# Kernel optimization log

Hardware: AMD Instinct MI355X
Metric: run time of the kernel (lower is better)

## Reference

```python
import jax, jax.numpy as jnp
import numpy as np

MARGIN = 0.3
N = 16384


def setup_inputs() -> dict:
    key = jax.random.key(0)
    k1, k2 = jax.random.split(key)
    inputs = jax.random.normal(k1, (N,), dtype=jnp.float32)
    targets = jax.random.randint(k2, (N,), 0, 2, dtype=jnp.int64)
    return {"inputs": inputs, "targets": targets}


def reference(inputs, targets):
    # Original: a = inputs[targets==1], b = inputs[targets==0];
    # all pairs (i, j): MarginRankingLoss(sigmoid(a_i), sigmoid(b_j), y=1)
    #   = mean_ij relu(margin - (sigmoid(a_i) - sigmoid(b_j)))
    # Expressed as a masked N x N broadcast so shapes stay static (jit-safe).
    s = jax.nn.sigmoid(inputs)  # [N]
    pos = (targets == 1)        # anchors-positive side
    neg = (targets == 0)        # negative side
    # hinge[i, j] = relu(margin - (s_i - s_j)) for pos i, neg j
    hinge = jax.nn.relu(MARGIN - (s[:, None] - s[None, :]))  # [N, N]
    mask = pos[:, None] & neg[None, :]                        # [N, N]
    num_pairs = jnp.sum(pos) * jnp.sum(neg)
    total = jnp.sum(jnp.where(mask, hinge, 0.0))
    return total / num_pairs.astype(s.dtype)
```

## Files before the change

### kernel.cpp

```cpp
#include <hip/hip_runtime.h>
#include <hip/hip_bf16.h>
#include <math.h>

#define MARGIN 0.3f
#define PAIR_BLOCKS 512


__global__ __launch_bounds__(256) void prep_compact_kernel(
        const float* __restrict__ inputs,
        const int* __restrict__ targets,
        float* __restrict__ a,
        float* __restrict__ b,
        unsigned int* __restrict__ pos_count,
        unsigned int* __restrict__ neg_count,
        int n) {
    __shared__ unsigned int wPos[4], wNeg[4];
    __shared__ unsigned int basePos, baseNeg;
    const int tid = threadIdx.x;
    const int i = blockIdx.x * 256 + tid;
    const bool valid = (i < n);
    float x = valid ? inputs[i] : 0.0f;
    int t = valid ? targets[i] : -1;
    float s = 1.0f / (1.0f + expf(-x));
    bool isPos = valid && (t == 1);
    bool isNeg = valid && (t == 0);

    unsigned long long mP = __ballot(isPos);
    unsigned long long mN = __ballot(isNeg);
    int lane = tid & 63, wave = tid >> 6;
    unsigned long long below = (1ull << lane) - 1ull;
    unsigned int pPre = (unsigned int)__popcll(mP & below);
    unsigned int nPre = (unsigned int)__popcll(mN & below);
    if (lane == 0) { wPos[wave] = (unsigned int)__popcll(mP);
                     wNeg[wave] = (unsigned int)__popcll(mN); }
    __syncthreads();
    if (tid == 0) {
        unsigned int tp = wPos[0] + wPos[1] + wPos[2] + wPos[3];
        unsigned int tn = wNeg[0] + wNeg[1] + wNeg[2] + wNeg[3];
        basePos = atomicAdd(pos_count, tp);
        baseNeg = atomicAdd(neg_count, tn);
    }
    __syncthreads();
    unsigned int wOffP = 0, wOffN = 0;
    for (int w = 0; w < wave; w++) { wOffP += wPos[w]; wOffN += wNeg[w]; }
    if (isPos) a[basePos + wOffP + pPre] = s;
    if (isNeg) b[baseNeg + wOffN + nPre] = MARGIN + s;
}

__global__ __launch_bounds__(256) void pair_reduce_kernel(
        const float* __restrict__ a,
        const float* __restrict__ b,
        const unsigned int* __restrict__ pos_count,
        const unsigned int* __restrict__ neg_count,
        double* __restrict__ total,
        unsigned int* __restrict__ done,
        float* __restrict__ out) {
    const int tid = threadIdx.x;
    const unsigned int P = *pos_count;
    const unsigned int Q = *neg_count;
    const unsigned int tilesI = (P + 511u) / 512u;
    const unsigned int tilesJ = (Q + 255u) / 256u;
    const unsigned int numTiles = tilesI * tilesJ;

    __shared__ float4 bs4[64];
    __shared__ double wsum[4];
    float* bs = (float*)bs4;

    double dlocal = 0.0;

    for (unsigned int tile = blockIdx.x; tile < numTiles; tile += gridDim.x) {
        unsigned int ti = tile / tilesJ;
        unsigned int tj = tile - ti * tilesJ;

        unsigned int j = tj * 256u + tid;
        bs[tid] = (j < Q) ? b[j] : -1e30f;

        unsigned int i0 = ti * 512u + tid;
        float a0 = (i0        < P) ? a[i0]       : 1e30f;
        float a1 = (i0 + 256u < P) ? a[i0 + 256] : 1e30f;
        __syncthreads();

        float c0 = 0.0f, c1 = 0.0f;
        #pragma unroll 8
        for (int q4 = 0; q4 < 64; q4++) {
            float4 b4 = bs4[q4];
            c0 += fmaxf(b4.x - a0, 0.0f);
            c0 += fmaxf(b4.y - a0, 0.0f);
            c0 += fmaxf(b4.z - a0, 0.0f);
            c0 += fmaxf(b4.w - a0, 0.0f);
            c1 += fmaxf(b4.x - a1, 0.0f);
            c1 += fmaxf(b4.y - a1, 0.0f);
            c1 += fmaxf(b4.z - a1, 0.0f);
            c1 += fmaxf(b4.w - a1, 0.0f);
        }
        dlocal += (double)c0 + (double)c1;
        __syncthreads();
    }

    for (int off = 32; off > 0; off >>= 1)
        dlocal += __shfl_down(dlocal, off, 64);

    int lane = tid & 63, wave = tid >> 6;
    if (lane == 0) wsum[wave] = dlocal;
    __syncthreads();
    if (tid == 0) {
        double bsum = wsum[0] + wsum[1] + wsum[2] + wsum[3];
        atomicAdd(total, bsum);
        __threadfence();
        unsigned int prev = atomicAdd(done, 1u);
        if (prev == gridDim.x - 1) {
            __threadfence();
            double T = atomicAdd(total, 0.0);
            double PQ = (double)P * (double)Q;
            out[0] = (PQ > 0.0) ? (float)(T / PQ) : 0.0f;
        }
    }
}

extern "C" void kernel_launch(void* const* d_in, const int* in_sizes, int n_in,
                              void* d_out, int out_size, void* d_ws, size_t ws_size,
                              hipStream_t stream) {
    const float* inputs  = (const float*)d_in[0];
    const int*   targets = (const int*)d_in[1];
    float* out = (float*)d_out;
    int n = in_sizes[0];

    char* ws = (char*)d_ws;
    double*       total     = (double*)(ws + 0);
    unsigned int* pos_count = (unsigned int*)(ws + 8);
    unsigned int* neg_count = (unsigned int*)(ws + 12);
    unsigned int* done      = (unsigned int*)(ws + 16);
    float*        a         = (float*)(ws + 32);
    float*        b         = (float*)(ws + 32 + (size_t)n * sizeof(float));

    hipMemsetAsync(d_ws, 0, 32, stream);

    int blocks = (n + 255) / 256;
    prep_compact_kernel<<<blocks, 256, 0, stream>>>(
        inputs, targets, a, b, pos_count, neg_count, n);

    pair_reduce_kernel<<<PAIR_BLOCKS, 256, 0, stream>>>(
        a, b, pos_count, neg_count, total, done, out);
}
```

Before: 76.66 us.

## Fuse compaction and pair reduction into one cooperative kernel with per-chunk compaction

Replaces the memset and the two kernel launches with one cooperative kernel that uses grid-wide syncs. Compaction no longer uses global atomics. Each 256-element chunk is compacted in place, padded with sentinels, and its counts are stored per chunk. The pair stage then walks every chunk tile, trimming the inner loop to the live negative count and skipping waves with no live rows. A deterministic partials reduction replaces the atomic total. This removes launch, memset and atomic overhead, but it creates more tiles with block syncs and adds the cost of grid synchronisation.

```diff
diff --git a/kernel.cpp b/kernel.cpp
--- a/kernel.cpp
+++ b/kernel.cpp
@@ -1,118 +1,134 @@
 #include <hip/hip_runtime.h>
-#include <hip/hip_bf16.h>
+#include <hip/hip_cooperative_groups.h>
 #include <math.h>
 
+namespace cg = cooperative_groups;
+
 #define MARGIN 0.3f
-#define PAIR_BLOCKS 512
+#define GRID_BLOCKS 512
+#define BLOCK 256
 
 
-__global__ __launch_bounds__(256) void prep_compact_kernel(
+__global__ __launch_bounds__(BLOCK) void fused_triplet_kernel(
         const float* __restrict__ inputs,
         const int* __restrict__ targets,
         float* __restrict__ a,
         float* __restrict__ b,
-        unsigned int* __restrict__ pos_count,
-        unsigned int* __restrict__ neg_count,
+        unsigned int* __restrict__ pc,
+        unsigned int* __restrict__ nc,
+        double* __restrict__ partials,
+        float* __restrict__ out,
         int n) {
-    __shared__ unsigned int wPos[4], wNeg[4];
-    __shared__ unsigned int basePos, baseNeg;
+    cg::grid_group grid = cg::this_grid();
     const int tid = threadIdx.x;
-    const int i = blockIdx.x * 256 + tid;
-    const bool valid = (i < n);
-    float x = valid ? inputs[i] : 0.0f;
-    int t = valid ? targets[i] : -1;
-    float s = 1.0f / (1.0f + expf(-x));
-    bool isPos = valid && (t == 1);
-    bool isNeg = valid && (t == 0);
+    const int lane = tid & 63, wave = tid >> 6;
+    const int numChunks = (n + 255) / 256;
+    const int Npad = numChunks * 256;
 
-    unsigned long long mP = __ballot(isPos);
-    unsigned long long mN = __ballot(isNeg);
-    int lane = tid & 63, wave = tid >> 6;
-    unsigned long long below = (1ull << lane) - 1ull;
-    unsigned int pPre = (unsigned int)__popcll(mP & below);
-    unsigned int nPre = (unsigned int)__popcll(mN & below);
-    if (lane == 0) { wPos[wave] = (unsigned int)__popcll(mP);
-                     wNeg[wave] = (unsigned int)__popcll(mN); }
-    __syncthreads();
-    if (tid == 0) {
-        unsigned int tp = wPos[0] + wPos[1] + wPos[2] + wPos[3];
-        unsigned int tn = wNeg[0] + wNeg[1] + wNeg[2] + wNeg[3];
-        basePos = atomicAdd(pos_count, tp);
-        baseNeg = atomicAdd(neg_count, tn);
+    __shared__ unsigned int wP[4], wN[4];
+    __shared__ float4 bs4[64];
+    float* bs = (float*)bs4;
+    __shared__ double wsum[4];
+    __shared__ unsigned int fp[4], fq[4];
+
+    for (int c = blockIdx.x; c < numChunks; c += gridDim.x) {
+        const int base = c * 256;
+        const int i = base + tid;
+        const bool valid = (i < n);
+        float x = valid ? inputs[i] : 0.0f;
+        int   t = valid ? targets[i] : -1;
+        float s = 1.0f / (1.0f + expf(-x));
+        bool isPos = valid && (t == 1);
+        bool isNeg = valid && (t == 0);
+
+        a[base + tid] = 1e30f;
+        b[base + tid] = -1e30f;
+
+        unsigned long long mP = __ballot(isPos);
+        unsigned long long mN = __ballot(isNeg);
+        unsigned long long below = (1ull << lane) - 1ull;
+        unsigned int pPre = (unsigned int)__popcll(mP & below);
+        unsigned int nPre = (unsigned int)__popcll(mN & below);
+        if (lane == 0) { wP[wave] = (unsigned int)__popcll(mP);
+                         wN[wave] = (unsigned int)__popcll(mN); }
+        __syncthreads();
+        unsigned int offP = 0, offN = 0;
+        for (int w = 0; w < wave; w++) { offP += wP[w]; offN += wN[w]; }
+        if (isPos) a[base + offP + pPre] = s;
+        if (isNeg) b[base + offN + nPre] = MARGIN + s;
+        if (tid == 0) {
+            pc[c] = wP[0] + wP[1] + wP[2] + wP[3];
+            nc[c] = wN[0] + wN[1] + wN[2] + wN[3];
+        }
+        __syncthreads();
     }
-    __syncthreads();
-    unsigned int wOffP = 0, wOffN = 0;
-    for (int w = 0; w < wave; w++) { wOffP += wPos[w]; wOffN += wNeg[w]; }
-    if (isPos) a[basePos + wOffP + pPre] = s;
-    if (isNeg) b[baseNeg + wOffN + nPre] = MARGIN + s;
-}
+    __threadfence();
+    grid.sync();
 
-__global__ __launch_bounds__(256) void pair_reduce_kernel(
-        const float* __restrict__ a,
-        const float* __restrict__ b,
-        const unsigned int* __restrict__ pos_count,
-        const unsigned int* __restrict__ neg_count,
-        double* __restrict__ total,
-        unsigned int* __restrict__ done,
-        float* __restrict__ out) {
-    const int tid = threadIdx.x;
-    const unsigned int P = *pos_count;
-    const unsigned int Q = *neg_count;
-    const unsigned int tilesI = (P + 511u) / 512u;
-    const unsigned int tilesJ = (Q + 255u) / 256u;
-    const unsigned int numTiles = tilesI * tilesJ;
-
-    __shared__ float4 bs4[64];
-    __shared__ double wsum[4];
-    float* bs = (float*)bs4;
-
+    const int tilesI = (Npad + 511) / 512;
+    const int tilesJ = numChunks;
+    const int numTiles = tilesI * tilesJ;
     double dlocal = 0.0;
 
-    for (unsigned int tile = blockIdx.x; tile < numTiles; tile += gridDim.x) {
-        unsigned int ti = tile / tilesJ;
-        unsigned int tj = tile - ti * tilesJ;
+    for (int tile = blockIdx.x; tile < numTiles; tile += gridDim.x) {
+        int ti = tile / tilesJ;
+        int tj = tile - ti * tilesJ;
 
-        unsigned int j = tj * 256u + tid;
-        bs[tid] = (j < Q) ? b[j] : -1e30f;
-
-        unsigned int i0 = ti * 512u + tid;
-        float a0 = (i0        < P) ? a[i0]       : 1e30f;
-        float a1 = (i0 + 256u < P) ? a[i0 + 256] : 1e30f;
+        __syncthreads();
+        bs[tid] = b[tj * 256 + tid];
         __syncthreads();
 
-        float c0 = 0.0f, c1 = 0.0f;
-        #pragma unroll 8
-        for (int q4 = 0; q4 < 64; q4++) {
-            float4 b4 = bs4[q4];
-            c0 += fmaxf(b4.x - a0, 0.0f);
-            c0 += fmaxf(b4.y - a0, 0.0f);
-            c0 += fmaxf(b4.z - a0, 0.0f);
-            c0 += fmaxf(b4.w - a0, 0.0f);
-            c1 += fmaxf(b4.x - a1, 0.0f);
-            c1 += fmaxf(b4.y - a1, 0.0f);
-            c1 += fmaxf(b4.z - a1, 0.0f);
-            c1 += fmaxf(b4.w - a1, 0.0f);
+        unsigned int ncv = nc[tj];
+        int i0 = ti * 512 + tid;
+        float a0 = (i0        < Npad) ? a[i0]       : 1e30f;
+        float a1 = (i0 + 256  < Npad) ? a[i0 + 256] : 1e30f;
+
+        bool rowLive = (a0 < 1e29f) || (a1 < 1e29f);
+        if (__any(rowLive)) {
+            int nq4 = (int)((ncv + 3u) >> 2);
+            float c0 = 0.0f, c1 = 0.0f;
+            #pragma unroll 4
+            for (int q4 = 0; q4 < nq4; q4++) {
+                float4 b4 = bs4[q4];
+                c0 += fmaxf(b4.x - a0, 0.0f);
+                c0 += fmaxf(b4.y - a0, 0.0f);
+                c0 += fmaxf(b4.z - a0, 0.0f);
+                c0 += fmaxf(b4.w - a0, 0.0f);
+                c1 += fmaxf(b4.x - a1, 0.0f);
+                c1 += fmaxf(b4.y - a1, 0.0f);
+                c1 += fmaxf(b4.z - a1, 0.0f);
+                c1 += fmaxf(b4.w - a1, 0.0f);
+            }
+            dlocal += (double)c0 + (double)c1;
         }
-        dlocal += (double)c0 + (double)c1;
-        __syncthreads();
     }
 
     for (int off = 32; off > 0; off >>= 1)
         dlocal += __shfl_down(dlocal, off, 64);
-
-    int lane = tid & 63, wave = tid >> 6;
     if (lane == 0) wsum[wave] = dlocal;
     __syncthreads();
-    if (tid == 0) {
-        double bsum = wsum[0] + wsum[1] + wsum[2] + wsum[3];
-        atomicAdd(total, bsum);
-        __threadfence();
-        unsigned int prev = atomicAdd(done, 1u);
-        if (prev == gridDim.x - 1) {
-            __threadfence();
-            double T = atomicAdd(total, 0.0);
-            double PQ = (double)P * (double)Q;
-            out[0] = (PQ > 0.0) ? (float)(T / PQ) : 0.0f;
+    if (tid == 0)
+        partials[blockIdx.x] = wsum[0] + wsum[1] + wsum[2] + wsum[3];
+    __threadfence();
+    grid.sync();
+
+    if (blockIdx.x == 0) {
+        double tsum = 0.0;
+        unsigned int p = 0, q = 0;
+        for (int k = tid; k < (int)gridDim.x; k += 256) tsum += partials[k];
+        for (int k = tid; k < numChunks; k += 256) { p += pc[k]; q += nc[k]; }
+        for (int off = 32; off > 0; off >>= 1) {
+            tsum += __shfl_down(tsum, off, 64);
+            p    += __shfl_down(p, off, 64);
+            q    += __shfl_down(q, off, 64);
+        }
+        if (lane == 0) { wsum[wave] = tsum; fp[wave] = p; fq[wave] = q; }
+        __syncthreads();
+        if (tid == 0) {
+            double T = wsum[0] + wsum[1] + wsum[2] + wsum[3];
+            double P = (double)(fp[0] + fp[1] + fp[2] + fp[3]);
+            double Q = (double)(fq[0] + fq[1] + fq[2] + fq[3]);
+            out[0] = (P > 0.0 && Q > 0.0) ? (float)(T / (P * Q)) : 0.0f;
         }
     }
 }
@@ -125,20 +141,18 @@
     float* out = (float*)d_out;
     int n = in_sizes[0];
 
+    int numChunks = (n + 255) / 256;
+    int Npad = numChunks * 256;
+
     char* ws = (char*)d_ws;
-    double*       total     = (double*)(ws + 0);
-    unsigned int* pos_count = (unsigned int*)(ws + 8);
-    unsigned int* neg_count = (unsigned int*)(ws + 12);
-    unsigned int* done      = (unsigned int*)(ws + 16);
-    float*        a         = (float*)(ws + 32);
-    float*        b         = (float*)(ws + 32 + (size_t)n * sizeof(float));
+    float*        a        = (float*)ws;
+    float*        b        = a + Npad;
+    unsigned int* pc       = (unsigned int*)(b + Npad);
+    unsigned int* nc       = pc + numChunks;
+    double*       partials = (double*)(ws + (size_t)8 * Npad + (size_t)8 * numChunks);
 
-    hipMemsetAsync(d_ws, 0, 32, stream);
-
-    int blocks = (n + 255) / 256;
-    prep_compact_kernel<<<blocks, 256, 0, stream>>>(
-        inputs, targets, a, b, pos_count, neg_count, n);
-
-    pair_reduce_kernel<<<PAIR_BLOCKS, 256, 0, stream>>>(
-        a, b, pos_count, neg_count, total, done, out);
+    void* args[] = { (void*)&inputs, (void*)&targets, (void*)&a, (void*)&b,
+                     (void*)&pc, (void*)&nc, (void*)&partials, (void*)&out, (void*)&n };
+    hipLaunchCooperativeKernel((const void*)fused_triplet_kernel,
+                               dim3(GRID_BLOCKS), dim3(BLOCK), args, 0, stream);
 }
```

Result: slower. 222.2 us (+189.9%).
